# Performance work log

Measured on AMD Instinct MI355X. Metric: run time of the kernel, lower is better.

Reference implementation:

```python
import jax, jax.numpy as jnp
import numpy as np

B, T, C, H = 2, 2048, 1024, 16
D = C // H  # head dim = 64
EPS = 1e-6  # kernel adds 1e-6 to softmax denominator


def setup_inputs() -> dict:
    key = jax.random.key(0)
    k1, k2, k3, k4, k5 = jax.random.split(key, 5)
    s = 1.0 / np.sqrt(C)
    return {
        "x": jax.random.normal(k1, (B, T, C), dtype=jnp.float32),
        "w_attn": jax.random.normal(k2, (3 * C, C), dtype=jnp.float32) * s,
        "b_attn": jax.random.normal(k3, (3 * C,), dtype=jnp.float32) * 0.02,
        "w_proj": jax.random.normal(k4, (C, C), dtype=jnp.float32) * s,
        "b_proj": jax.random.normal(k5, (C,), dtype=jnp.float32) * 0.02,
    }


def reference(x, w_attn, b_attn, w_proj, b_proj):
    b, t, c = x.shape
    qkv = x @ w_attn.T + b_attn                      # [B,T,3C]
    q, k, v = jnp.split(qkv, 3, axis=2)
    # [B,T,C] -> [B,H,T,D]
    q = q.reshape(b, t, H, D).transpose(0, 2, 1, 3)
    k = k.reshape(b, t, H, D).transpose(0, 2, 1, 3)
    v = v.reshape(b, t, H, D).transpose(0, 2, 1, 3)
    scale = 1.0 / np.sqrt(D)
    att = jnp.einsum("bhid,bhjd->bhij", q, k) * scale  # [B,H,T,T]
    causal = jnp.tril(jnp.ones((t, t), dtype=bool))
    att = jnp.where(causal, att, -jnp.inf)
    # softmax matching the HIP kernel: denom has +1e-6
    m = jnp.max(att, axis=-1, keepdims=True)
    e = jnp.exp(att - m)                             # masked entries -> 0
    p = e / (jnp.sum(e, axis=-1, keepdims=True) + EPS)
    y = jnp.einsum("bhij,bhjd->bhid", p, v)          # [B,H,T,D]
    y = y.transpose(0, 2, 1, 3).reshape(b, t, c)     # [B,T,C]
    return y @ w_proj.T + b_proj
```

## Files before the change

### kernel.cpp

```cpp
#include <hip/hip_runtime.h>

#define B_ 2
#define T_ 2048
#define C_ 1024
#define H_ 16
#define D_ 64

typedef __bf16 bf16x8 __attribute__((ext_vector_type(8)));
typedef float f32x4 __attribute__((ext_vector_type(4)));

__device__ __forceinline__ unsigned short f2bf(float f) {
  unsigned u = __float_as_uint(f);
  unsigned r = (u + 0x7fffu + ((u >> 16) & 1u)) >> 16;
  return (unsigned short)r;
}

#define NX 1048576
#define NWA 786432
#define NWP 262144
__global__ __launch_bounds__(256) void convert_all(
    const float* __restrict__ x, const float* __restrict__ wa,
    const float* __restrict__ wp, unsigned short* __restrict__ xb,
    unsigned short* __restrict__ wab, unsigned short* __restrict__ wpb) {
  int i = blockIdx.x * 256 + threadIdx.x;
  const float* s; unsigned short* d; int j;
  if (i < NX)            { s = x;  d = xb;  j = i; }
  else if (i < NX + NWA) { s = wa; d = wab; j = i - NX; }
  else                   { s = wp; d = wpb; j = i - NX - NWA; }
  float4 v = ((const float4*)s)[j];
  ushort4 u;
  u.x = f2bf(v.x); u.y = f2bf(v.y); u.z = f2bf(v.z); u.w = f2bf(v.w);
  ((ushort4*)d)[j] = u;
}

__global__ __launch_bounds__(256) void gemm_bt(
    const unsigned short* __restrict__ A,
    const unsigned short* __restrict__ Bm,
    const float* __restrict__ bias,
    int M, int N, int K, int mode,
    float* __restrict__ outf,
    unsigned short* __restrict__ qb,
    unsigned short* __restrict__ kb,
    unsigned short* __restrict__ vb) {
  __shared__ unsigned short As[128 * 64];
  __shared__ unsigned short Bs[128 * 64];

  const int tid  = threadIdx.x;
  const int lane = tid & 63;
  const int wave = tid >> 6;
  const int quad = lane >> 4;
  const int l16  = lane & 15;
  const int q4   = quad * 4;

  const int bm = blockIdx.y * 128;
  const int bn = blockIdx.x * 128;
  const int wm = (wave >> 1) * 64;
  const int wn = (wave & 1) * 64;

  f32x4 acc[4][4] = {};

  const int srow8 = lane >> 3;
  const int scol  = ((lane & 7) ^ srow8) * 8;
  const int srow  = wave * 8 + srow8;

  for (int k0 = 0; k0 < K; k0 += 64) {
#pragma unroll
    for (int c = 0; c < 4; ++c) {
      const int r = c * 32 + srow;
      const unsigned short* ga = A  + (size_t)(bm + r) * K + (k0 + scol);
      const unsigned short* gb = Bm + (size_t)(bn + r) * K + (k0 + scol);
      unsigned short* la = &As[(c * 32 + wave * 8) * 64];
      unsigned short* lb = &Bs[(c * 32 + wave * 8) * 64];
      __builtin_amdgcn_global_load_lds(
          (__attribute__((address_space(1))) unsigned int*)ga,
          (__attribute__((address_space(3))) unsigned int*)la, 16, 0, 0);
      __builtin_amdgcn_global_load_lds(
          (__attribute__((address_space(1))) unsigned int*)gb,
          (__attribute__((address_space(3))) unsigned int*)lb, 16, 0, 0);
    }
    __syncthreads();
#pragma unroll
    for (int ks = 0; ks < 2; ++ks) {
      bf16x8 af[4], bfr[4];
#pragma unroll
      for (int i = 0; i < 4; ++i)
        af[i] = *(const bf16x8*)&As[(wm + i * 16 + l16) * 64 +
                                    (((ks * 4 + quad) ^ (l16 & 7)) * 8)];
#pragma unroll
      for (int j = 0; j < 4; ++j)
        bfr[j] = *(const bf16x8*)&Bs[(wn + j * 16 + l16) * 64 +
                                     (((ks * 4 + quad) ^ (l16 & 7)) * 8)];
#pragma unroll
      for (int i = 0; i < 4; ++i)
#pragma unroll
        for (int j = 0; j < 4; ++j)
          acc[i][j] = __builtin_amdgcn_mfma_f32_16x16x32_bf16(af[i], bfr[j], acc[i][j], 0, 0, 0);
    }
    __syncthreads();
  }

#pragma unroll
  for (int j = 0; j < 4; ++j) {
    const int gn = bn + wn + j * 16 + l16;
    const float bv = bias[gn];
    if (mode == 0) {
#pragma unroll
      for (int i = 0; i < 4; ++i)
#pragma unroll
        for (int r = 0; r < 4; ++r) {
          const int gm = bm + wm + i * 16 + q4 + r;
          outf[(size_t)gm * N + gn] = acc[i][j][r] + bv;
        }
    } else {
      const int which = gn >> 10;
      const int cc = gn & 1023;
      const int h = cc >> 6, d = cc & 63;
      if (which == 2) {
#pragma unroll
        for (int i = 0; i < 4; ++i) {
          const int gm0 = bm + wm + i * 16 + q4;
          const int b = gm0 >> 11, t0 = gm0 & 2047;
          ushort4 u;
          u.x = f2bf(acc[i][j][0] + bv);
          u.y = f2bf(acc[i][j][1] + bv);
          u.z = f2bf(acc[i][j][2] + bv);
          u.w = f2bf(acc[i][j][3] + bv);
          *(ushort4*)&vb[(((size_t)(b * H_ + h) * D_) + d) * T_ + t0] = u;
        }
      } else {
        const float sc = (which == 0) ? 0.125f : 1.0f;
        unsigned short* dst = (which == 0) ? qb : kb;
#pragma unroll
        for (int i = 0; i < 4; ++i)
#pragma unroll
          for (int r = 0; r < 4; ++r) {
            const int gm = bm + wm + i * 16 + q4 + r;
            const int b = gm >> 11, t = gm & 2047;
            dst[(((size_t)(b * H_ + h) * T_) + t) * D_ + d] = f2bf((acc[i][j][r] + bv) * sc);
          }
      }
    }
  }
}

__global__ __launch_bounds__(256, 2) void attn_mfma(
    const unsigned short* __restrict__ Qb,
    const unsigned short* __restrict__ Kb,
    const unsigned short* __restrict__ Vtg,
    unsigned short* __restrict__ Yb,
    unsigned short* __restrict__ op,
    float* __restrict__ lp) {
  __shared__ unsigned short Ks[64 * 64];
  __shared__ unsigned short Vt[64 * 64];
  __shared__ unsigned short Pw[4][32 * 64];

  const int tid  = threadIdx.x;
  const int lane = tid & 63;
  const int wave = tid >> 6;
  const int quad = lane >> 4;
  const int l16  = lane & 15;
  const int q4   = quad * 4;
  const int sw   = (l16 & 7);

  const int id = blockIdx.x;
  const int bh = id / 40;
  const int w  = id - bh * 40;
  int qt, chunk, nsplits;
  if (w < 4)       { qt = w;                 chunk = 0;            nsplits = 1; }
  else if (w < 12) { qt = 4 + ((w - 4) >> 1); chunk = (w - 4) & 1;  nsplits = 2; }
  else if (w < 24) { qt = 8 + (w - 12) / 3;  chunk = (w - 12) % 3; nsplits = 3; }
  else             { qt = 12 + ((w - 24) >> 2); chunk = (w - 24) & 3; nsplits = 4; }

  const int tiles_total = 2 * qt + 2;
  const int tpc = (tiles_total + nsplits - 1) / nsplits;
  const int t0 = chunk * tpc;
  const int t1 = min(t0 + tpc, tiles_total);

  const int b = bh >> 4, h = bh & 15;
  const size_t base = (size_t)bh * T_ * D_;
  const int wq = qt * 128 + wave * 32;
  const int wt1 = min(t1, (wq + 95) >> 6);

  bf16x8 qf[2][2];
#pragma unroll
  for (int nt = 0; nt < 2; ++nt)
#pragma unroll
    for (int ks = 0; ks < 2; ++ks)
      qf[nt][ks] = *(const bf16x8*)(Qb + base + (size_t)(wq + nt * 16 + l16) * 64 +
                                    ks * 32 + quad * 8);

  f32x4 o[4][2] = {};
  float l2[2] = {0.f, 0.f};

  const int srow8 = lane >> 3;
  const int satom = ((lane & 7) ^ srow8) * 8;

  for (int kt = t0; kt < t1; ++kt) {
    const int kt0 = kt * 64;
    __syncthreads();
#pragma unroll
    for (int c = 0; c < 2; ++c) {
      const int row = wave * 16 + c * 8 + srow8;
      const unsigned short* gk = Kb  + base + (size_t)(kt0 + row) * 64 + satom;
      const unsigned short* gv = Vtg + base + (size_t)row * T_ + kt0 + satom;
      unsigned short* lk = &Ks[(wave * 16 + c * 8) * 64];
      unsigned short* lv = &Vt[(wave * 16 + c * 8) * 64];
      __builtin_amdgcn_global_load_lds(
          (__attribute__((address_space(1))) unsigned int*)gk,
          (__attribute__((address_space(3))) unsigned int*)lk, 16, 0, 0);
      __builtin_amdgcn_global_load_lds(
          (__attribute__((address_space(1))) unsigned int*)gv,
          (__attribute__((address_space(3))) unsigned int*)lv, 16, 0, 0);
    }
    __syncthreads();

    if (kt < wt1) {
      f32x4 s[4][2] = {};
#pragma unroll
      for (int ks = 0; ks < 2; ++ks) {
        bf16x8 kf[4];
#pragma unroll
        for (int mt = 0; mt < 4; ++mt)
          kf[mt] = *(const bf16x8*)&Ks[(mt * 16 + l16) * 64 +
                                       (((ks * 4 + quad) ^ sw) * 8)];
#pragma unroll
        for (int mt = 0; mt < 4; ++mt)
#pragma unroll
          for (int nt = 0; nt < 2; ++nt)
            s[mt][nt] = __builtin_amdgcn_mfma_f32_16x16x32_bf16(kf[mt], qf[nt][ks],
                                                                s[mt][nt], 0, 0, 0);
      }
      if (kt0 + 63 > wq) {
#pragma unroll
        for (int mt = 0; mt < 4; ++mt)
#pragma unroll
          for (int nt = 0; nt < 2; ++nt)
#pragma unroll
            for (int r = 0; r < 4; ++r)
              if (kt0 + mt * 16 + q4 + r > wq + nt * 16 + l16) s[mt][nt][r] = -1e30f;
      }
#pragma unroll
      for (int nt = 0; nt < 2; ++nt) {
        float ps = 0.f;
#pragma unroll
        for (int mt = 0; mt < 4; ++mt) {
          float p0 = __expf(s[mt][nt][0]);
          float p1 = __expf(s[mt][nt][1]);
          float p2 = __expf(s[mt][nt][2]);
          float p3 = __expf(s[mt][nt][3]);
          ps += (p0 + p1) + (p2 + p3);
          unsigned lo = __builtin_amdgcn_perm(__float_as_uint(p1) + 0x8000u,
                                              __float_as_uint(p0) + 0x8000u,
                                              0x07060302u);
          unsigned hi = __builtin_amdgcn_perm(__float_as_uint(p3) + 0x8000u,
                                              __float_as_uint(p2) + 0x8000u,
                                              0x07060302u);
          uint2 pk; pk.x = lo; pk.y = hi;
          const int atom = (2 * mt + (quad >> 1)) ^ sw;
          *(uint2*)&Pw[wave][(nt * 16 + l16) * 64 + atom * 8 + (quad & 1) * 4] = pk;
        }
        l2[nt] += ps;
      }
#pragma unroll
      for (int ks = 0; ks < 2; ++ks) {
        bf16x8 vf[4], pf[2];
#pragma unroll
        for (int dt = 0; dt < 4; ++dt)
          vf[dt] = *(const bf16x8*)&Vt[(dt * 16 + l16) * 64 +
                                       (((ks * 4 + quad) ^ sw) * 8)];
#pragma unroll
        for (int nt = 0; nt < 2; ++nt)
          pf[nt] = *(const bf16x8*)&Pw[wave][(nt * 16 + l16) * 64 +
                                            (((ks * 4 + quad) ^ sw) * 8)];
#pragma unroll
        for (int dt = 0; dt < 4; ++dt)
#pragma unroll
          for (int nt = 0; nt < 2; ++nt)
            o[dt][nt] = __builtin_amdgcn_mfma_f32_16x16x32_bf16(vf[dt], pf[nt],
                                                                o[dt][nt], 0, 0, 0);
      }
    }
  }

#pragma unroll
  for (int nt = 0; nt < 2; ++nt) {
    float l = l2[nt];
    l += __shfl_xor(l, 16);
    l += __shfl_xor(l, 32);
    const int qloc = wave * 32 + nt * 16 + l16;
    if (nsplits == 1) {
      const float inv = 1.f / (l + 1e-6f);
      const int q = qt * 128 + qloc;
#pragma unroll
      for (int dt = 0; dt < 4; ++dt) {
        ushort4 u;
        u.x = f2bf(o[dt][nt][0] * inv);
        u.y = f2bf(o[dt][nt][1] * inv);
        u.z = f2bf(o[dt][nt][2] * inv);
        u.w = f2bf(o[dt][nt][3] * inv);
        *(ushort4*)&Yb[((size_t)(b * T_ + q)) * C_ + h * 64 + dt * 16 + q4] = u;
      }
    } else {
      if (quad == 0) lp[(size_t)id * 128 + qloc] = l;
#pragma unroll
      for (int dt = 0; dt < 4; ++dt) {
        ushort4 u;
        u.x = f2bf(o[dt][nt][0]);
        u.y = f2bf(o[dt][nt][1]);
        u.z = f2bf(o[dt][nt][2]);
        u.w = f2bf(o[dt][nt][3]);
        *(ushort4*)&op[(size_t)id * 8192 + (size_t)qloc * 64 + dt * 16 + q4] = u;
      }
    }
  }
}

__global__ __launch_bounds__(256) void attn_combine(
    const unsigned short* __restrict__ op, const float* __restrict__ lp,
    unsigned short* __restrict__ Yb) {
  const int cb = blockIdx.x;
  const int bh = cb / 12;
  const int qi = cb - bh * 12;
  const int qt = 4 + qi;
  int nsplits, pfx;
  if (qt < 8)       { nsplits = 2; pfx = 4 + 2 * (qt - 4); }
  else if (qt < 12) { nsplits = 3; pfx = 12 + 3 * (qt - 8); }
  else              { nsplits = 4; pfx = 24 + 4 * (qt - 12); }
  const int slot0 = bh * 40 + pfx;

  const int t = threadIdx.x;
  const int qloc = t >> 1;
  const int d0 = (t & 1) * 32;

  float l = 1e-6f;
  float acc[32];
#pragma unroll
  for (int i = 0; i < 32; ++i) acc[i] = 0.f;
  for (int s = 0; s < nsplits; ++s) {
    l += lp[(size_t)(slot0 + s) * 128 + qloc];
    const uint4* src = (const uint4*)(op + (size_t)(slot0 + s) * 8192 +
                                      (size_t)qloc * 64 + d0);
#pragma unroll
    for (int c = 0; c < 4; ++c) {
      uint4 v = src[c];
      acc[c*8+0] += __uint_as_float(v.x << 16);
      acc[c*8+1] += __uint_as_float(v.x & 0xffff0000u);
      acc[c*8+2] += __uint_as_float(v.y << 16);
      acc[c*8+3] += __uint_as_float(v.y & 0xffff0000u);
      acc[c*8+4] += __uint_as_float(v.z << 16);
      acc[c*8+5] += __uint_as_float(v.z & 0xffff0000u);
      acc[c*8+6] += __uint_as_float(v.w << 16);
      acc[c*8+7] += __uint_as_float(v.w & 0xffff0000u);
    }
  }
  const float inv = 1.f / l;
  const int b = bh >> 4, h = bh & 15;
  const int q = qt * 128 + qloc;
  uint4* dst = (uint4*)(Yb + ((size_t)(b * T_ + q)) * C_ + h * 64 + d0);
#pragma unroll
  for (int c = 0; c < 4; ++c) {
    uint4 v;
    v.x = (unsigned)f2bf(acc[c*8+0] * inv) | ((unsigned)f2bf(acc[c*8+1] * inv) << 16);
    v.y = (unsigned)f2bf(acc[c*8+2] * inv) | ((unsigned)f2bf(acc[c*8+3] * inv) << 16);
    v.z = (unsigned)f2bf(acc[c*8+4] * inv) | ((unsigned)f2bf(acc[c*8+5] * inv) << 16);
    v.w = (unsigned)f2bf(acc[c*8+6] * inv) | ((unsigned)f2bf(acc[c*8+7] * inv) << 16);
    dst[c] = v;
  }
}

extern "C" void kernel_launch(void* const* d_in, const int* in_sizes, int n_in,
                              void* d_out, int out_size, void* d_ws, size_t ws_size,
                              hipStream_t stream) {
  const float* x      = (const float*)d_in[0];
  const float* w_attn = (const float*)d_in[1];
  const float* b_attn = (const float*)d_in[2];
  const float* w_proj = (const float*)d_in[3];
  const float* b_proj = (const float*)d_in[4];
  float* out = (float*)d_out;

  char* ws = (char*)d_ws;
  unsigned short* xb  = (unsigned short*)ws;  ws += (size_t)4096 * 1024 * 2;
  unsigned short* wab = (unsigned short*)ws;  ws += (size_t)3072 * 1024 * 2;
  unsigned short* wpb = (unsigned short*)ws;  ws += (size_t)1024 * 1024 * 2;
  unsigned short* qb  = (unsigned short*)ws;  ws += (size_t)B_ * H_ * T_ * D_ * 2;
  unsigned short* kb  = (unsigned short*)ws;  ws += (size_t)B_ * H_ * T_ * D_ * 2;
  unsigned short* vb  = (unsigned short*)ws;  ws += (size_t)B_ * H_ * T_ * D_ * 2;
  unsigned short* yb  = (unsigned short*)ws;  ws += (size_t)4096 * 1024 * 2;
  unsigned short* op  = (unsigned short*)ws;  ws += (size_t)1280 * 128 * 64 * 2;
  float*          lp  = (float*)ws;           ws += (size_t)1280 * 128 * 4;
  (void)ws_size; (void)in_sizes; (void)n_in; (void)out_size;

  convert_all<<<8192, 256, 0, stream>>>(x, w_attn, w_proj, xb, wab, wpb);

  gemm_bt<<<dim3(24, 32), 256, 0, stream>>>(xb, wab, b_attn, 4096, 3072, 1024, 1,
                                            nullptr, qb, kb, vb);
  attn_mfma<<<1280, 256, 0, stream>>>(qb, kb, vb, yb, op, lp);
  attn_combine<<<384, 256, 0, stream>>>(op, lp, yb);
  gemm_bt<<<dim3(8, 32), 256, 0, stream>>>(yb, wpb, b_proj, 4096, 1024, 1024, 0,
                                           out, nullptr, nullptr, nullptr);
}
```

Before: 183.4 us.

## Double-buffer K/V tiles in attention and shrink per-wave P scratch

```diff
diff --git a/kernel.cpp b/kernel.cpp
--- a/kernel.cpp
+++ b/kernel.cpp
@@ -143,16 +143,16 @@
   }
 }
 
-__global__ __launch_bounds__(256, 2) void attn_mfma(
+__global__ __launch_bounds__(256, 4) void attn_mfma(
     const unsigned short* __restrict__ Qb,
     const unsigned short* __restrict__ Kb,
     const unsigned short* __restrict__ Vtg,
     unsigned short* __restrict__ Yb,
     unsigned short* __restrict__ op,
     float* __restrict__ lp) {
-  __shared__ unsigned short Ks[64 * 64];
-  __shared__ unsigned short Vt[64 * 64];
-  __shared__ unsigned short Pw[4][32 * 64];
+  __shared__ unsigned short Ks[2][64 * 64];
+  __shared__ unsigned short Vt[2][64 * 64];
+  __shared__ unsigned short Pn[4][16 * 64];
 
   const int tid  = threadIdx.x;
   const int lane = tid & 63;
@@ -195,24 +195,32 @@
   const int srow8 = lane >> 3;
   const int satom = ((lane & 7) ^ srow8) * 8;
 
+#define STAGE_TILE(KT, BUF)                                                      \
+  do {                                                                           \
+    const int kt0_ = (KT) * 64;                                                  \
+    _Pragma("unroll")                                                            \
+    for (int c = 0; c < 2; ++c) {                                                \
+      const int row = wave * 16 + c * 8 + srow8;                                 \
+      const unsigned short* gk = Kb  + base + (size_t)(kt0_ + row) * 64 + satom; \
+      const unsigned short* gv = Vtg + base + (size_t)row * T_ + kt0_ + satom;   \
+      __builtin_amdgcn_global_load_lds(                                          \
+          (__attribute__((address_space(1))) unsigned int*)gk,                   \
+          (__attribute__((address_space(3))) unsigned int*)                      \
+              &Ks[BUF][(wave * 16 + c * 8) * 64], 16, 0, 0);                     \
+      __builtin_amdgcn_global_load_lds(                                          \
+          (__attribute__((address_space(1))) unsigned int*)gv,                   \
+          (__attribute__((address_space(3))) unsigned int*)                      \
+              &Vt[BUF][(wave * 16 + c * 8) * 64], 16, 0, 0);                     \
+    }                                                                            \
+  } while (0)
+
+  STAGE_TILE(t0, t0 & 1);
+  __syncthreads();
+
   for (int kt = t0; kt < t1; ++kt) {
     const int kt0 = kt * 64;
-    __syncthreads();
-#pragma unroll
-    for (int c = 0; c < 2; ++c) {
-      const int row = wave * 16 + c * 8 + srow8;
-      const unsigned short* gk = Kb  + base + (size_t)(kt0 + row) * 64 + satom;
-      const unsigned short* gv = Vtg + base + (size_t)row * T_ + kt0 + satom;
-      unsigned short* lk = &Ks[(wave * 16 + c * 8) * 64];
-      unsigned short* lv = &Vt[(wave * 16 + c * 8) * 64];
-      __builtin_amdgcn_global_load_lds(
-          (__attribute__((address_space(1))) unsigned int*)gk,
-          (__attribute__((address_space(3))) unsigned int*)lk, 16, 0, 0);
-      __builtin_amdgcn_global_load_lds(
-          (__attribute__((address_space(1))) unsigned int*)gv,
-          (__attribute__((address_space(3))) unsigned int*)lv, 16, 0, 0);
-    }
-    __syncthreads();
+    const int cur = kt & 1;
+    if (kt + 1 < t1) STAGE_TILE(kt + 1, (kt + 1) & 1);
 
     if (kt < wt1) {
       f32x4 s[4][2] = {};
@@ -221,8 +229,8 @@
         bf16x8 kf[4];
 #pragma unroll
         for (int mt = 0; mt < 4; ++mt)
-          kf[mt] = *(const bf16x8*)&Ks[(mt * 16 + l16) * 64 +
-                                       (((ks * 4 + quad) ^ sw) * 8)];
+          kf[mt] = *(const bf16x8*)&Ks[cur][(mt * 16 + l16) * 64 +
+                                           (((ks * 4 + quad) ^ sw) * 8)];
 #pragma unroll
         for (int mt = 0; mt < 4; ++mt)
 #pragma unroll
@@ -257,30 +265,28 @@
                                               0x07060302u);
           uint2 pk; pk.x = lo; pk.y = hi;
           const int atom = (2 * mt + (quad >> 1)) ^ sw;
-          *(uint2*)&Pw[wave][(nt * 16 + l16) * 64 + atom * 8 + (quad & 1) * 4] = pk;
+          *(uint2*)&Pn[wave][l16 * 64 + atom * 8 + (quad & 1) * 4] = pk;
         }
         l2[nt] += ps;
-      }
-#pragma unroll
-      for (int ks = 0; ks < 2; ++ks) {
-        bf16x8 vf[4], pf[2];
-#pragma unroll
-        for (int dt = 0; dt < 4; ++dt)
-          vf[dt] = *(const bf16x8*)&Vt[(dt * 16 + l16) * 64 +
-                                       (((ks * 4 + quad) ^ sw) * 8)];
-#pragma unroll
-        for (int nt = 0; nt < 2; ++nt)
-          pf[nt] = *(const bf16x8*)&Pw[wave][(nt * 16 + l16) * 64 +
-                                            (((ks * 4 + quad) ^ sw) * 8)];
-#pragma unroll
-        for (int dt = 0; dt < 4; ++dt)
-#pragma unroll
-          for (int nt = 0; nt < 2; ++nt)
-            o[dt][nt] = __builtin_amdgcn_mfma_f32_16x16x32_bf16(vf[dt], pf[nt],
+#pragma unroll
+        for (int ks = 0; ks < 2; ++ks) {
+          bf16x8 pf = *(const bf16x8*)&Pn[wave][l16 * 64 +
+                                               (((ks * 4 + quad) ^ sw) * 8)];
+          bf16x8 vf[4];
+#pragma unroll
+          for (int dt = 0; dt < 4; ++dt)
+            vf[dt] = *(const bf16x8*)&Vt[cur][(dt * 16 + l16) * 64 +
+                                             (((ks * 4 + quad) ^ sw) * 8)];
+#pragma unroll
+          for (int dt = 0; dt < 4; ++dt)
+            o[dt][nt] = __builtin_amdgcn_mfma_f32_16x16x32_bf16(vf[dt], pf,
                                                                 o[dt][nt], 0, 0, 0);
-      }
-    }
-  }
+        }
+      }
+    }
+    __syncthreads();
+  }
+#undef STAGE_TILE
 
 #pragma unroll
   for (int nt = 0; nt < 2; ++nt) {
```

After: 210.4 us. +14.7%, slower.

## Rebalance attention split-K schedule and shrink per-wave P buffer in LDS

Applied to the files above, without the earlier changes.

```diff
diff --git a/kernel.cpp b/kernel.cpp
--- a/kernel.cpp
+++ b/kernel.cpp
@@ -152,7 +152,7 @@
     float* __restrict__ lp) {
   __shared__ unsigned short Ks[64 * 64];
   __shared__ unsigned short Vt[64 * 64];
-  __shared__ unsigned short Pw[4][32 * 64];
+  __shared__ unsigned short Pn[4][16 * 64];
 
   const int tid  = threadIdx.x;
   const int lane = tid & 63;
@@ -163,13 +163,15 @@
   const int sw   = (l16 & 7);
 
   const int id = blockIdx.x;
-  const int bh = id / 40;
-  const int w  = id - bh * 40;
-  int qt, chunk, nsplits;
-  if (w < 4)       { qt = w;                 chunk = 0;            nsplits = 1; }
-  else if (w < 12) { qt = 4 + ((w - 4) >> 1); chunk = (w - 4) & 1;  nsplits = 2; }
-  else if (w < 24) { qt = 8 + (w - 12) / 3;  chunk = (w - 12) % 3; nsplits = 3; }
-  else             { qt = 12 + ((w - 24) >> 2); chunk = (w - 24) & 3; nsplits = 4; }
+  const int bh = id / 51;
+  const int w  = id - bh * 51;
+  int qt = 0, nsplits = 1, pfx = 0;
+  for (int q = 0; q < 16; ++q) {
+    const int n = (2 * q + 7) / 6;
+    if (w < pfx + n) { qt = q; nsplits = n; break; }
+    pfx += n;
+  }
+  const int chunk = w - pfx;
 
   const int tiles_total = 2 * qt + 2;
   const int tpc = (tiles_total + nsplits - 1) / nsplits;
@@ -257,27 +259,23 @@
                                               0x07060302u);
           uint2 pk; pk.x = lo; pk.y = hi;
           const int atom = (2 * mt + (quad >> 1)) ^ sw;
-          *(uint2*)&Pw[wave][(nt * 16 + l16) * 64 + atom * 8 + (quad & 1) * 4] = pk;
+          *(uint2*)&Pn[wave][l16 * 64 + atom * 8 + (quad & 1) * 4] = pk;
         }
         l2[nt] += ps;
-      }
-#pragma unroll
-      for (int ks = 0; ks < 2; ++ks) {
-        bf16x8 vf[4], pf[2];
-#pragma unroll
-        for (int dt = 0; dt < 4; ++dt)
-          vf[dt] = *(const bf16x8*)&Vt[(dt * 16 + l16) * 64 +
-                                       (((ks * 4 + quad) ^ sw) * 8)];
-#pragma unroll
-        for (int nt = 0; nt < 2; ++nt)
-          pf[nt] = *(const bf16x8*)&Pw[wave][(nt * 16 + l16) * 64 +
-                                            (((ks * 4 + quad) ^ sw) * 8)];
-#pragma unroll
-        for (int dt = 0; dt < 4; ++dt)
-#pragma unroll
-          for (int nt = 0; nt < 2; ++nt)
-            o[dt][nt] = __builtin_amdgcn_mfma_f32_16x16x32_bf16(vf[dt], pf[nt],
+#pragma unroll
+        for (int ks = 0; ks < 2; ++ks) {
+          bf16x8 pf = *(const bf16x8*)&Pn[wave][l16 * 64 +
+                                               (((ks * 4 + quad) ^ sw) * 8)];
+          bf16x8 vf[4];
+#pragma unroll
+          for (int dt = 0; dt < 4; ++dt)
+            vf[dt] = *(const bf16x8*)&Vt[(dt * 16 + l16) * 64 +
+                                         (((ks * 4 + quad) ^ sw) * 8)];
+#pragma unroll
+          for (int dt = 0; dt < 4; ++dt)
+            o[dt][nt] = __builtin_amdgcn_mfma_f32_16x16x32_bf16(vf[dt], pf,
                                                                 o[dt][nt], 0, 0, 0);
+        }
       }
     }
   }
@@ -319,14 +317,15 @@
     const unsigned short* __restrict__ op, const float* __restrict__ lp,
     unsigned short* __restrict__ Yb) {
   const int cb = blockIdx.x;
-  const int bh = cb / 12;
-  const int qi = cb - bh * 12;
-  const int qt = 4 + qi;
-  int nsplits, pfx;
-  if (qt < 8)       { nsplits = 2; pfx = 4 + 2 * (qt - 4); }
-  else if (qt < 12) { nsplits = 3; pfx = 12 + 3 * (qt - 8); }
-  else              { nsplits = 4; pfx = 24 + 4 * (qt - 12); }
-  const int slot0 = bh * 40 + pfx;
+  const int bh = cb / 13;
+  const int qt = 3 + (cb - bh * 13);
+  int pfx = 0;
+  for (int q = 0; q < 16; ++q) {
+    if (q == qt) break;
+    pfx += (2 * q + 7) / 6;
+  }
+  const int nsplits = (2 * qt + 7) / 6;
+  const int slot0 = bh * 51 + pfx;
 
   const int t = threadIdx.x;
   const int qloc = t >> 1;
@@ -386,16 +385,16 @@
   unsigned short* kb  = (unsigned short*)ws;  ws += (size_t)B_ * H_ * T_ * D_ * 2;
   unsigned short* vb  = (unsigned short*)ws;  ws += (size_t)B_ * H_ * T_ * D_ * 2;
   unsigned short* yb  = (unsigned short*)ws;  ws += (size_t)4096 * 1024 * 2;
-  unsigned short* op  = (unsigned short*)ws;  ws += (size_t)1280 * 128 * 64 * 2;
-  float*          lp  = (float*)ws;           ws += (size_t)1280 * 128 * 4;
+  unsigned short* op  = (unsigned short*)ws;  ws += (size_t)1632 * 128 * 64 * 2;
+  float*          lp  = (float*)ws;           ws += (size_t)1632 * 128 * 4;
   (void)ws_size; (void)in_sizes; (void)n_in; (void)out_size;
 
   convert_all<<<8192, 256, 0, stream>>>(x, w_attn, w_proj, xb, wab, wpb);
 
   gemm_bt<<<dim3(24, 32), 256, 0, stream>>>(xb, wab, b_attn, 4096, 3072, 1024, 1,
                                             nullptr, qb, kb, vb);
-  attn_mfma<<<1280, 256, 0, stream>>>(qb, kb, vb, yb, op, lp);
-  attn_combine<<<384, 256, 0, stream>>>(op, lp, yb);
+  attn_mfma<<<1632, 256, 0, stream>>>(qb, kb, vb, yb, op, lp);
+  attn_combine<<<416, 256, 0, stream>>>(op, lp, yb);
   gemm_bt<<<dim3(8, 32), 256, 0, stream>>>(yb, wpb, b_proj, 4096, 1024, 1024, 0,
                                            out, nullptr, nullptr, nullptr);
 }
```

Result: slower. 189.0 us (+3.0%).
